# Kernel optimization log

Measured on AMD Instinct MI355X. Metric: run time of the kernel, lower is better.

Reference implementation:

```python
import jax, jax.numpy as jnp
import numpy as np

COMMITMENT_COST = 0.25


def setup_inputs() -> dict:
    key = jax.random.key(0)
    k1, k2 = jax.random.split(key)
    B, H, W, D, K = 64, 32, 32, 64, 1024
    x = jax.random.normal(k1, (B, H, W, D), dtype=jnp.float32)
    # variance_scaling(fan_in=D, uniform) ~ U(-sqrt(3/D), sqrt(3/D)); plain normal*scale is fine for a reference
    embeddings = jax.random.uniform(k2, (D, K), dtype=jnp.float32,
                                    minval=-np.sqrt(3.0 / D), maxval=np.sqrt(3.0 / D))
    return {"x": x, "embeddings": embeddings}


def reference(x, embeddings):
    D = embeddings.shape[0]
    K = embeddings.shape[1]
    flat = x.reshape(-1, D)                                   # [N, D]
    # squared euclidean distance: ||f||^2 - 2 f.E + ||e||^2 -> [N, K]
    distance = (jnp.sum(flat ** 2, axis=1, keepdims=True)
                - 2.0 * jnp.matmul(flat, embeddings)
                + jnp.sum(embeddings ** 2, axis=0, keepdims=True))
    encoding_indices_flat = jnp.argmax(-distance, axis=1)     # [N]
    encodings = jax.nn.one_hot(encoding_indices_flat, K, dtype=distance.dtype)  # [N, K]
    encoding_indices = encoding_indices_flat.reshape(x.shape[:-1])
    # quantize: gather rows of E^T -> same shape as x
    quantized = jnp.take(embeddings.T, encoding_indices, axis=0)
    e_latent_loss = jnp.mean((jax.lax.stop_gradient(quantized) - x) ** 2)
    q_latent_loss = jnp.mean((quantized - jax.lax.stop_gradient(x)) ** 2)
    loss = q_latent_loss + COMMITMENT_COST * e_latent_loss
    quantized_st = x + jax.lax.stop_gradient(quantized - x)   # straight-through
    avg_probs = jnp.mean(encodings, axis=0)                   # [K]
    perplexity = jnp.exp(-jnp.sum(avg_probs * jnp.log(avg_probs + 1e-10)))
    return quantized_st, loss, perplexity, encoding_indices
```

## Files before the change

### kernel.cpp

```cpp
#include <hip/hip_runtime.h>
#include <math.h>


typedef __attribute__((ext_vector_type(8))) short short8v;
typedef __attribute__((ext_vector_type(4))) float float4v;
typedef unsigned short u16;
typedef unsigned int u32;

constexpr int D = 64;
constexpr int K = 1024;
constexpr int NPTS = 65536;
constexpr long QOFF = (long)NPTS * D;
constexpr float BIAS = 24.0f;
constexpr float GATE = 5e-3f;

constexpr size_t OFF_LOSS = 0;
constexpr size_t OFF_CNT  = 256;
constexpr size_t OFF_EC   = OFF_CNT + 4096;
constexpr size_t OFF_ECB  = OFF_EC + 4096;
constexpr size_t OFF_ET   = OFF_ECB + 4096;
constexpr size_t OFF_H2   = OFF_ET + (size_t)K * D * 4;
constexpr size_t OFF_L2   = OFF_H2 + (size_t)K * D * 2;
constexpr size_t WS_ZERO  = OFF_CNT + 4096;

__device__ __forceinline__ float med3(float a, float b, float c) {
  return __builtin_amdgcn_fmed3f(a, b, c);
}
__device__ __forceinline__ u16 bf16rtn(float x) {
  u32 u = __float_as_uint(x);
  return (u16)((u + 0x7fffu + ((u >> 16) & 1u)) >> 16);
}
__device__ __forceinline__ float bf2f(u16 h) {
  return __uint_as_float(((u32)h) << 16);
}

__global__ __launch_bounds__(256) void prep_norm(const float* __restrict__ E,
                                                 float* __restrict__ eC,
                                                 float* __restrict__ eCb) {
  int k = blockIdx.x * 256 + threadIdx.x;
  float c = __fmul_rn(E[k], E[k]);
#pragma unroll
  for (int d = 1; d < D; ++d) {
    float v = E[d * K + k];
    c = __fadd_rn(c, __fmul_rn(v, v));
  }
  eC[k] = c;
  eCb[k] = c + BIAS;
}

__global__ __launch_bounds__(256) void prep_conv(const float* __restrict__ E,
                                                 float* __restrict__ Et,
                                                 u16* __restrict__ h2,
                                                 u16* __restrict__ l2) {
  int gid = blockIdx.x * 256 + threadIdx.x;
  int k = gid & 1023;
  int dg = gid >> 10;
#pragma unroll
  for (int i = 0; i < 4; ++i) {
    int d = dg * 4 + i;
    float v = E[d * K + k];
    Et[(size_t)k * 64 + d] = v;
    float m2 = -2.0f * v;
    u16 h = bf16rtn(m2);
    u16 l = bf16rtn(m2 - bf2f(h));
    h2[(size_t)k * 64 + d] = h;
    l2[(size_t)k * 64 + d] = l;
  }
}

__global__ __launch_bounds__(256) void vq_main(const float* __restrict__ x,
                                               const float* __restrict__ E,
                                               const u16* __restrict__ h2g,
                                               const u16* __restrict__ l2g,
                                               const float* __restrict__ eC,
                                               const float* __restrict__ eCb,
                                               const float* __restrict__ Etg,
                                               float* __restrict__ out,
                                               double* __restrict__ lossSum,
                                               int* __restrict__ counts) {
  __shared__ __align__(16) u16 hA[128 * 72];
  __shared__ __align__(16) u16 lA[128 * 72];
  __shared__ __align__(16) float ecb[128];
  __shared__ __align__(16) float topbuf[256 * 4];
  __shared__ int bkbuf[128];

  const int tid = threadIdx.x;
  const int w = tid >> 6;
  const int lane = tid & 63;
  const int col = lane & 15;
  const int quad = lane >> 4;
  const int blockBase = blockIdx.x * 128;
  const float INF = __builtin_inff();

  short8v Bh[2][2], Bl[2][2];
#pragma unroll
  for (int pt = 0; pt < 2; ++pt) {
    const float* xp = x + (size_t)(blockBase + w * 32 + pt * 16 + col) * 64;
#pragma unroll
    for (int s = 0; s < 2; ++s) {
      const float4* src = (const float4*)(xp + s * 32 + quad * 8);
      float4 a = src[0], b = src[1];
      float xs[8] = {a.x, a.y, a.z, a.w, b.x, b.y, b.z, b.w};
      short8v hf, lf;
#pragma unroll
      for (int j = 0; j < 8; ++j) {
        u16 h = bf16rtn(xs[j]);
        hf[j] = (short)h;
        lf[j] = (short)bf16rtn(xs[j] - bf2f(h));
      }
      Bh[pt][s] = hf;
      Bl[pt][s] = lf;
    }
  }

  float b1[2] = {INF, INF}, b2[2] = {INF, INF};

  for (int ch = 0; ch < 8; ++ch) {
    const int kbase = ch * 128;
    __syncthreads();
#pragma unroll
    for (int i = 0; i < 4; ++i) {
      int idx = tid + i * 256;
      int k = idx >> 3, dg = idx & 7;
      *(float4*)&hA[k * 72 + dg * 8] =
          *(const float4*)&h2g[(size_t)(kbase + k) * 64 + dg * 8];
      *(float4*)&lA[k * 72 + dg * 8] =
          *(const float4*)&l2g[(size_t)(kbase + k) * 64 + dg * 8];
    }
    if (tid < 32) *(float4*)&ecb[tid * 4] = *(const float4*)&eCb[kbase + tid * 4];
    __syncthreads();

#pragma unroll
    for (int ct = 0; ct < 8; ++ct) {
      const int rowbase = (ct * 16 + col) * 72;
      short8v Ah0 = *(const short8v*)&hA[rowbase + quad * 8];
      short8v Ah1 = *(const short8v*)&hA[rowbase + 32 + quad * 8];
      short8v Al0 = *(const short8v*)&lA[rowbase + quad * 8];
      short8v Al1 = *(const short8v*)&lA[rowbase + 32 + quad * 8];
      float4v Ci = *(const float4v*)&ecb[ct * 16 + quad * 4];
#pragma unroll
      for (int pt = 0; pt < 2; ++pt) {
        float4v C = Ci;
        C = __builtin_amdgcn_mfma_f32_16x16x32_bf16(Ah0, Bh[pt][0], C, 0, 0, 0);
        C = __builtin_amdgcn_mfma_f32_16x16x32_bf16(Ah1, Bh[pt][1], C, 0, 0, 0);
        C = __builtin_amdgcn_mfma_f32_16x16x32_bf16(Al0, Bh[pt][0], C, 0, 0, 0);
        C = __builtin_amdgcn_mfma_f32_16x16x32_bf16(Al1, Bh[pt][1], C, 0, 0, 0);
        C = __builtin_amdgcn_mfma_f32_16x16x32_bf16(Ah0, Bl[pt][0], C, 0, 0, 0);
        C = __builtin_amdgcn_mfma_f32_16x16x32_bf16(Ah1, Bl[pt][1], C, 0, 0, 0);
#pragma unroll
        for (int r = 0; r < 4; ++r) {
          u32 u = (__float_as_uint(C[r]) & 0xffffff00u) |
                  (u32)(ch * 32 + ct * 4 + r);
          float v = __uint_as_float(u);
          float pb = b1[pt];
          b1[pt] = fminf(pb, v);
          b2[pt] = med3(pb, b2[pt], v);
        }
      }
    }
  }

  topbuf[tid * 4 + 0] = b1[0];
  topbuf[tid * 4 + 1] = b2[0];
  topbuf[tid * 4 + 2] = b1[1];
  topbuf[tid * 4 + 3] = b2[1];
  __syncthreads();

  if (tid < 128) {
    const int mw = tid >> 5, mpt = (tid >> 4) & 1, mcol = tid & 15;
    float cv[8];
    int cq[8];
    float mv0 = INF, mv1 = INF;
    int q0 = 0;
#pragma unroll
    for (int q = 0; q < 4; ++q) {
      int lbase = (mw * 64 + q * 16 + mcol) * 4 + mpt * 2;
#pragma unroll
      for (int j = 0; j < 2; ++j) {
        float v = topbuf[lbase + j];
        cv[q * 2 + j] = v;
        cq[q * 2 + j] = q;
        if (v < mv0) { mv1 = mv0; mv0 = v; q0 = q; }
        else if (v < mv1) { mv1 = v; }
      }
    }
    u32 lb = __float_as_uint(mv0) & 255u;
    int bestk = (int)((lb >> 5) * 128 + ((lb >> 2) & 7) * 16 + q0 * 4 + (lb & 3));

    if (mv1 - mv0 < GATE) {
      const float* f = x + (size_t)(blockBase + tid) * 64;
      float r8[8];
#pragma unroll
      for (int j = 0; j < 8; ++j) { float fv = f[j]; r8[j] = __fmul_rn(fv, fv); }
#pragma unroll
      for (int i = 8; i < D; i += 8)
#pragma unroll
        for (int j = 0; j < 8; ++j) {
          float fv = f[i + j];
          r8[j] = __fadd_rn(r8[j], __fmul_rn(fv, fv));
        }
      float A = __fadd_rn(__fadd_rn(__fadd_rn(r8[0], r8[1]), __fadd_rn(r8[2], r8[3])),
                          __fadd_rn(__fadd_rn(r8[4], r8[5]), __fadd_rn(r8[6], r8[7])));
      float bd = INF;
      int bkk = K;
#pragma unroll
      for (int c = 0; c < 8; ++c) {
        u32 cb = __float_as_uint(cv[c]) & 255u;
        int k = (int)((cb >> 5) * 128 + ((cb >> 2) & 7) * 16 + cq[c] * 4 + (cb & 3));
        float m = 0.f;
#pragma unroll
        for (int d = 0; d < D; ++d) m = __fmaf_rn(f[d], E[d * K + k], m);
        float dist = __fadd_rn(__fsub_rn(A, __fmul_rn(2.f, m)), eC[k]);
        bool better = (dist < bd) || (dist == bd && k < bkk);
        bd = better ? dist : bd;
        bkk = better ? k : bkk;
      }
      bestk = bkk;
    }

    bkbuf[tid] = bestk;
    out[QOFF + 2 + blockBase + tid] = (float)bestk;
    atomicAdd(&counts[bestk], 1);
  }
  __syncthreads();

  const int pp = tid >> 1, half = tid & 1;
  const int bk = bkbuf[pp];
  const float4* et = (const float4*)(Etg + (size_t)bk * 64 + half * 32);
  const float4* xr = (const float4*)(x + (size_t)(blockBase + pp) * 64 + half * 32);
  float4* ov = (float4*)(out + (size_t)(blockBase + pp) * 64 + half * 32);
  float errs = 0.f;
#pragma unroll
  for (int i = 0; i < 8; ++i) {
    float4 qv = et[i];
    float4 xv = xr[i];
    float dx;
    dx = qv.x - xv.x; errs = fmaf(dx, dx, errs);
    dx = qv.y - xv.y; errs = fmaf(dx, dx, errs);
    dx = qv.z - xv.z; errs = fmaf(dx, dx, errs);
    dx = qv.w - xv.w; errs = fmaf(dx, dx, errs);
    ov[i] = qv;
  }
  double de = (double)errs;
#pragma unroll
  for (int off = 32; off > 0; off >>= 1) de += __shfl_down(de, off, 64);
  if (lane == 0) atomicAdd(lossSum, de);
}

__global__ __launch_bounds__(256) void vq_finalize(const double* __restrict__ lossSum,
                                                   const int* __restrict__ counts,
                                                   float* __restrict__ out) {
  __shared__ double sh[256];
  double ent = 0.0;
  for (int k = threadIdx.x; k < K; k += 256) {
    double pp = (double)counts[k] / (double)NPTS;
    ent += pp * log(pp + 1e-10);
  }
  sh[threadIdx.x] = ent;
  __syncthreads();
  for (int s = 128; s > 0; s >>= 1) {
    if (threadIdx.x < s) sh[threadIdx.x] += sh[threadIdx.x + s];
    __syncthreads();
  }
  if (threadIdx.x == 0) {
    out[QOFF + 0] = (float)(1.25 * (*lossSum) / (double)((long)NPTS * D));
    out[QOFF + 1] = (float)exp(-sh[0]);
  }
}

extern "C" void kernel_launch(void* const* d_in, const int* in_sizes, int n_in,
                              void* d_out, int out_size, void* d_ws, size_t ws_size,
                              hipStream_t stream) {
  const float* x = (const float*)d_in[0];
  const float* E = (const float*)d_in[1];
  float* out = (float*)d_out;

  char* ws = (char*)d_ws;
  double* lossSum = (double*)(ws + OFF_LOSS);
  int* counts = (int*)(ws + OFF_CNT);
  float* eC = (float*)(ws + OFF_EC);
  float* eCb = (float*)(ws + OFF_ECB);
  float* Etg = (float*)(ws + OFF_ET);
  u16* h2g = (u16*)(ws + OFF_H2);
  u16* l2g = (u16*)(ws + OFF_L2);

  hipMemsetAsync(d_ws, 0, WS_ZERO, stream);

  prep_norm<<<K / 256, 256, 0, stream>>>(E, eC, eCb);
  prep_conv<<<(K * 16) / 256, 256, 0, stream>>>(E, Etg, h2g, l2g);
  vq_main<<<NPTS / 128, 256, 0, stream>>>(x, E, h2g, l2g, eC, eCb, Etg, out,
                                          lossSum, counts);
  vq_finalize<<<1, 256, 0, stream>>>(lossSum, counts, out);
}
```

Baseline: 134.7 us.

## Use single fp16 MFMA pass with wider rescoring gate, drop LDS staging

Replaces the split bf16 hi/lo three-term product (6 MFMAs per tile) with a single fp16 product (2 MFMAs). The top-2 rescoring gate is widened to absorb the larger rounding error. Codebook tiles are now read straight from global/L2 instead of being staged through LDS with barriers, and the two prep kernels are merged into one. This cuts matrix-core work, LDS traffic and a kernel launch. The risk is more exact-rescore fallbacks and less coalesced per-lane global loads.

```diff
diff --git a/kernel.cpp b/kernel.cpp
--- a/kernel.cpp
+++ b/kernel.cpp
@@ -2,7 +2,7 @@
 #include <math.h>
 
 
-typedef __attribute__((ext_vector_type(8))) short short8v;
+typedef __attribute__((ext_vector_type(8))) _Float16 half8v;
 typedef __attribute__((ext_vector_type(4))) float float4v;
 typedef unsigned short u16;
 typedef unsigned int u32;
@@ -12,75 +12,58 @@
 constexpr int NPTS = 65536;
 constexpr long QOFF = (long)NPTS * D;
 constexpr float BIAS = 24.0f;
-constexpr float GATE = 5e-3f;
+constexpr float GATE = 2e-2f;
 
 constexpr size_t OFF_LOSS = 0;
 constexpr size_t OFF_CNT  = 256;
-constexpr size_t OFF_EC   = OFF_CNT + 4096;
-constexpr size_t OFF_ECB  = OFF_EC + 4096;
-constexpr size_t OFF_ET   = OFF_ECB + 4096;
-constexpr size_t OFF_H2   = OFF_ET + (size_t)K * D * 4;
-constexpr size_t OFF_L2   = OFF_H2 + (size_t)K * D * 2;
-constexpr size_t WS_ZERO  = OFF_CNT + 4096;
+constexpr size_t OFF_EC   = 4352;
+constexpr size_t OFF_ECB  = 8448;
+constexpr size_t OFF_ET   = 12544;
+constexpr size_t OFF_H16  = OFF_ET + (size_t)K * D * 4;
+constexpr size_t WS_ZERO  = 4352;
 
 __device__ __forceinline__ float med3(float a, float b, float c) {
   return __builtin_amdgcn_fmed3f(a, b, c);
 }
-__device__ __forceinline__ u16 bf16rtn(float x) {
-  u32 u = __float_as_uint(x);
-  return (u16)((u + 0x7fffu + ((u >> 16) & 1u)) >> 16);
-}
-__device__ __forceinline__ float bf2f(u16 h) {
-  return __uint_as_float(((u32)h) << 16);
-}
-
-__global__ __launch_bounds__(256) void prep_norm(const float* __restrict__ E,
-                                                 float* __restrict__ eC,
-                                                 float* __restrict__ eCb) {
-  int k = blockIdx.x * 256 + threadIdx.x;
-  float c = __fmul_rn(E[k], E[k]);
-#pragma unroll
-  for (int d = 1; d < D; ++d) {
-    float v = E[d * K + k];
-    c = __fadd_rn(c, __fmul_rn(v, v));
-  }
-  eC[k] = c;
-  eCb[k] = c + BIAS;
-}
-
-__global__ __launch_bounds__(256) void prep_conv(const float* __restrict__ E,
-                                                 float* __restrict__ Et,
-                                                 u16* __restrict__ h2,
-                                                 u16* __restrict__ l2) {
-  int gid = blockIdx.x * 256 + threadIdx.x;
-  int k = gid & 1023;
-  int dg = gid >> 10;
-#pragma unroll
-  for (int i = 0; i < 4; ++i) {
-    int d = dg * 4 + i;
-    float v = E[d * K + k];
-    Et[(size_t)k * 64 + d] = v;
-    float m2 = -2.0f * v;
-    u16 h = bf16rtn(m2);
-    u16 l = bf16rtn(m2 - bf2f(h));
-    h2[(size_t)k * 64 + d] = h;
-    l2[(size_t)k * 64 + d] = l;
+
+__global__ __launch_bounds__(256) void prep(const float* __restrict__ E,
+                                            float* __restrict__ eC,
+                                            float* __restrict__ eCb,
+                                            float* __restrict__ Et,
+                                            _Float16* __restrict__ h16) {
+  const int gid = blockIdx.x * 256 + threadIdx.x;
+  const int d = gid >> 8;
+  const int k0 = (gid & 255) * 4;
+  float4 v = *(const float4*)&E[d * K + k0];
+  Et[(size_t)(k0 + 0) * 64 + d] = v.x;
+  Et[(size_t)(k0 + 1) * 64 + d] = v.y;
+  Et[(size_t)(k0 + 2) * 64 + d] = v.z;
+  Et[(size_t)(k0 + 3) * 64 + d] = v.w;
+  h16[(size_t)(k0 + 0) * 64 + d] = (_Float16)(-2.0f * v.x);
+  h16[(size_t)(k0 + 1) * 64 + d] = (_Float16)(-2.0f * v.y);
+  h16[(size_t)(k0 + 2) * 64 + d] = (_Float16)(-2.0f * v.z);
+  h16[(size_t)(k0 + 3) * 64 + d] = (_Float16)(-2.0f * v.w);
+  if (gid < K) {
+    float c = __fmul_rn(E[gid], E[gid]);
+#pragma unroll
+    for (int dd = 1; dd < D; ++dd) {
+      float e = E[dd * K + gid];
+      c = __fadd_rn(c, __fmul_rn(e, e));
+    }
+    eC[gid] = c;
+    eCb[gid] = c + BIAS;
   }
 }
 
 __global__ __launch_bounds__(256) void vq_main(const float* __restrict__ x,
                                                const float* __restrict__ E,
-                                               const u16* __restrict__ h2g,
-                                               const u16* __restrict__ l2g,
+                                               const _Float16* __restrict__ h16,
                                                const float* __restrict__ eC,
                                                const float* __restrict__ eCb,
                                                const float* __restrict__ Etg,
                                                float* __restrict__ out,
                                                double* __restrict__ lossSum,
                                                int* __restrict__ counts) {
-  __shared__ __align__(16) u16 hA[128 * 72];
-  __shared__ __align__(16) u16 lA[128 * 72];
-  __shared__ __align__(16) float ecb[128];
   __shared__ __align__(16) float topbuf[256 * 4];
   __shared__ int bkbuf[128];
 
@@ -92,7 +75,7 @@
   const int blockBase = blockIdx.x * 128;
   const float INF = __builtin_inff();
 
-  short8v Bh[2][2], Bl[2][2];
+  half8v Bf[2][2];
 #pragma unroll
   for (int pt = 0; pt < 2; ++pt) {
     const float* xp = x + (size_t)(blockBase + w * 32 + pt * 16 + col) * 64;
@@ -100,53 +83,31 @@
     for (int s = 0; s < 2; ++s) {
       const float4* src = (const float4*)(xp + s * 32 + quad * 8);
       float4 a = src[0], b = src[1];
-      float xs[8] = {a.x, a.y, a.z, a.w, b.x, b.y, b.z, b.w};
-      short8v hf, lf;
-#pragma unroll
-      for (int j = 0; j < 8; ++j) {
-        u16 h = bf16rtn(xs[j]);
-        hf[j] = (short)h;
-        lf[j] = (short)bf16rtn(xs[j] - bf2f(h));
-      }
-      Bh[pt][s] = hf;
-      Bl[pt][s] = lf;
+      half8v hf;
+      hf[0] = (_Float16)a.x; hf[1] = (_Float16)a.y;
+      hf[2] = (_Float16)a.z; hf[3] = (_Float16)a.w;
+      hf[4] = (_Float16)b.x; hf[5] = (_Float16)b.y;
+      hf[6] = (_Float16)b.z; hf[7] = (_Float16)b.w;
+      Bf[pt][s] = hf;
     }
   }
 
   float b1[2] = {INF, INF}, b2[2] = {INF, INF};
 
+#pragma unroll 2
   for (int ch = 0; ch < 8; ++ch) {
-    const int kbase = ch * 128;
-    __syncthreads();
-#pragma unroll
-    for (int i = 0; i < 4; ++i) {
-      int idx = tid + i * 256;
-      int k = idx >> 3, dg = idx & 7;
-      *(float4*)&hA[k * 72 + dg * 8] =
-          *(const float4*)&h2g[(size_t)(kbase + k) * 64 + dg * 8];
-      *(float4*)&lA[k * 72 + dg * 8] =
-          *(const float4*)&l2g[(size_t)(kbase + k) * 64 + dg * 8];
-    }
-    if (tid < 32) *(float4*)&ecb[tid * 4] = *(const float4*)&eCb[kbase + tid * 4];
-    __syncthreads();
-
 #pragma unroll
     for (int ct = 0; ct < 8; ++ct) {
-      const int rowbase = (ct * 16 + col) * 72;
-      short8v Ah0 = *(const short8v*)&hA[rowbase + quad * 8];
-      short8v Ah1 = *(const short8v*)&hA[rowbase + 32 + quad * 8];
-      short8v Al0 = *(const short8v*)&lA[rowbase + quad * 8];
-      short8v Al1 = *(const short8v*)&lA[rowbase + 32 + quad * 8];
-      float4v Ci = *(const float4v*)&ecb[ct * 16 + quad * 4];
+      const int krow = ch * 128 + ct * 16;
+      const _Float16* arow = h16 + (size_t)(krow + col) * 64 + quad * 8;
+      half8v A0 = *(const half8v*)arow;
+      half8v A1 = *(const half8v*)(arow + 32);
+      float4v Ci = *(const float4v*)&eCb[krow + quad * 4];
 #pragma unroll
       for (int pt = 0; pt < 2; ++pt) {
         float4v C = Ci;
-        C = __builtin_amdgcn_mfma_f32_16x16x32_bf16(Ah0, Bh[pt][0], C, 0, 0, 0);
-        C = __builtin_amdgcn_mfma_f32_16x16x32_bf16(Ah1, Bh[pt][1], C, 0, 0, 0);
-        C = __builtin_amdgcn_mfma_f32_16x16x32_bf16(Al0, Bh[pt][0], C, 0, 0, 0);
-        C = __builtin_amdgcn_mfma_f32_16x16x32_bf16(Al1, Bh[pt][1], C, 0, 0, 0);
-        C = __builtin_amdgcn_mfma_f32_16x16x32_bf16(Ah0, Bl[pt][0], C, 0, 0, 0);
-        C = __builtin_amdgcn_mfma_f32_16x16x32_bf16(Ah1, Bl[pt][1], C, 0, 0, 0);
+        C = __builtin_amdgcn_mfma_f32_16x16x32_f16(A0, Bf[pt][0], C, 0, 0, 0);
+        C = __builtin_amdgcn_mfma_f32_16x16x32_f16(A1, Bf[pt][1], C, 0, 0, 0);
 #pragma unroll
         for (int r = 0; r < 4; ++r) {
           u32 u = (__float_as_uint(C[r]) & 0xffffff00u) |
@@ -281,14 +242,12 @@
   float* eC = (float*)(ws + OFF_EC);
   float* eCb = (float*)(ws + OFF_ECB);
   float* Etg = (float*)(ws + OFF_ET);
-  u16* h2g = (u16*)(ws + OFF_H2);
-  u16* l2g = (u16*)(ws + OFF_L2);
+  _Float16* h16 = (_Float16*)(ws + OFF_H16);
 
   hipMemsetAsync(d_ws, 0, WS_ZERO, stream);
 
-  prep_norm<<<K / 256, 256, 0, stream>>>(E, eC, eCb);
-  prep_conv<<<(K * 16) / 256, 256, 0, stream>>>(E, Etg, h2g, l2g);
-  vq_main<<<NPTS / 128, 256, 0, stream>>>(x, E, h2g, l2g, eC, eCb, Etg, out,
+  prep<<<64, 256, 0, stream>>>(E, eC, eCb, Etg, h16);
+  vq_main<<<NPTS / 128, 256, 0, stream>>>(x, E, h16, eC, eCb, Etg, out,
                                           lossSum, counts);
   vq_finalize<<<1, 256, 0, stream>>>(lossSum, counts, out);
 }
```

Measured after the change: 171.4 us. 27.3% more time.

## Merge prep kernels and fold finalize into main via last-block atomic

Applied to the files above, without the earlier changes.

Combines the two codebook preparation kernels into one that reads E with float4 loads. It removes the separate finalize launch: each block bumps a done counter, and the last block computes the entropy/perplexity and the loss output. The exact-rescoring fallback now loads the point into registers once and reads codebook rows from the transposed Et copy instead of strided E columns. The aim is fewer kernel launches and cheaper tie-break rescoring, at the cost of a grid-completion atomic and a serial tail in the last block.

```diff
diff --git a/kernel.cpp b/kernel.cpp
--- a/kernel.cpp
+++ b/kernel.cpp
@@ -13,15 +13,17 @@
 constexpr long QOFF = (long)NPTS * D;
 constexpr float BIAS = 24.0f;
 constexpr float GATE = 5e-3f;
+constexpr int GRID = 512;
 
 constexpr size_t OFF_LOSS = 0;
-constexpr size_t OFF_CNT  = 256;
-constexpr size_t OFF_EC   = OFF_CNT + 4096;
-constexpr size_t OFF_ECB  = OFF_EC + 4096;
-constexpr size_t OFF_ET   = OFF_ECB + 4096;
+constexpr size_t OFF_DONE = 8;
+constexpr size_t OFF_CNT  = 16;
+constexpr size_t WS_ZERO  = 4112;
+constexpr size_t OFF_EC   = 4352;
+constexpr size_t OFF_ECB  = 8448;
+constexpr size_t OFF_ET   = 12544;
 constexpr size_t OFF_H2   = OFF_ET + (size_t)K * D * 4;
 constexpr size_t OFF_L2   = OFF_H2 + (size_t)K * D * 2;
-constexpr size_t WS_ZERO  = OFF_CNT + 4096;
 
 __device__ __forceinline__ float med3(float a, float b, float c) {
   return __builtin_amdgcn_fmed3f(a, b, c);
@@ -34,55 +36,55 @@
   return __uint_as_float(((u32)h) << 16);
 }
 
-__global__ __launch_bounds__(256) void prep_norm(const float* __restrict__ E,
-                                                 float* __restrict__ eC,
-                                                 float* __restrict__ eCb) {
-  int k = blockIdx.x * 256 + threadIdx.x;
-  float c = __fmul_rn(E[k], E[k]);
-#pragma unroll
-  for (int d = 1; d < D; ++d) {
-    float v = E[d * K + k];
-    c = __fadd_rn(c, __fmul_rn(v, v));
-  }
-  eC[k] = c;
-  eCb[k] = c + BIAS;
-}
-
-__global__ __launch_bounds__(256) void prep_conv(const float* __restrict__ E,
-                                                 float* __restrict__ Et,
-                                                 u16* __restrict__ h2,
-                                                 u16* __restrict__ l2) {
-  int gid = blockIdx.x * 256 + threadIdx.x;
-  int k = gid & 1023;
-  int dg = gid >> 10;
+__global__ __launch_bounds__(256) void prep(const float* __restrict__ E,
+                                            float* __restrict__ eC,
+                                            float* __restrict__ eCb,
+                                            float* __restrict__ Et,
+                                            u16* __restrict__ h2,
+                                            u16* __restrict__ l2) {
+  const int gid = blockIdx.x * 256 + threadIdx.x;
+  const int d = gid >> 8;
+  const int k0 = (gid & 255) * 4;
+  float4 v = *(const float4*)&E[d * K + k0];
 #pragma unroll
   for (int i = 0; i < 4; ++i) {
-    int d = dg * 4 + i;
-    float v = E[d * K + k];
-    Et[(size_t)k * 64 + d] = v;
-    float m2 = -2.0f * v;
+    int k = k0 + i;
+    float e = (i == 0) ? v.x : (i == 1) ? v.y : (i == 2) ? v.z : v.w;
+    Et[(size_t)k * 64 + d] = e;
+    float m2 = -2.0f * e;
     u16 h = bf16rtn(m2);
-    u16 l = bf16rtn(m2 - bf2f(h));
     h2[(size_t)k * 64 + d] = h;
-    l2[(size_t)k * 64 + d] = l;
+    l2[(size_t)k * 64 + d] = bf16rtn(m2 - bf2f(h));
+  }
+  if (gid < K) {
+    float c = __fmul_rn(E[gid], E[gid]);
+#pragma unroll
+    for (int dd = 1; dd < D; ++dd) {
+      float e = E[dd * K + gid];
+      c = __fadd_rn(c, __fmul_rn(e, e));
+    }
+    eC[gid] = c;
+    eCb[gid] = c + BIAS;
   }
 }
 
 __global__ __launch_bounds__(256) void vq_main(const float* __restrict__ x,
-                                               const float* __restrict__ E,
                                                const u16* __restrict__ h2g,
                                                const u16* __restrict__ l2g,
                                                const float* __restrict__ eC,
-                                               const float* __restrict__ eCb,
+                                               const float* __restrict__ eCbG,
                                                const float* __restrict__ Etg,
                                                float* __restrict__ out,
                                                double* __restrict__ lossSum,
-                                               int* __restrict__ counts) {
+                                               int* __restrict__ counts,
+                                               int* __restrict__ done) {
   __shared__ __align__(16) u16 hA[128 * 72];
   __shared__ __align__(16) u16 lA[128 * 72];
   __shared__ __align__(16) float ecb[128];
   __shared__ __align__(16) float topbuf[256 * 4];
   __shared__ int bkbuf[128];
+  __shared__ double shred[256];
+  __shared__ int lastFlag;
 
   const int tid = threadIdx.x;
   const int w = tid >> 6;
@@ -127,7 +129,7 @@
       *(float4*)&lA[k * 72 + dg * 8] =
           *(const float4*)&l2g[(size_t)(kbase + k) * 64 + dg * 8];
     }
-    if (tid < 32) *(float4*)&ecb[tid * 4] = *(const float4*)&eCb[kbase + tid * 4];
+    if (tid < 32) *(float4*)&ecb[tid * 4] = *(const float4*)&eCbG[kbase + tid * 4];
     __syncthreads();
 
 #pragma unroll
@@ -188,28 +190,41 @@
     int bestk = (int)((lb >> 5) * 128 + ((lb >> 2) & 7) * 16 + q0 * 4 + (lb & 3));
 
     if (mv1 - mv0 < GATE) {
-      const float* f = x + (size_t)(blockBase + tid) * 64;
+      const float4* fx = (const float4*)(x + (size_t)(blockBase + tid) * 64);
+      float fr[64];
+#pragma unroll
+      for (int i = 0; i < 16; ++i) {
+        float4 v = fx[i];
+        fr[4 * i + 0] = v.x; fr[4 * i + 1] = v.y;
+        fr[4 * i + 2] = v.z; fr[4 * i + 3] = v.w;
+      }
       float r8[8];
 #pragma unroll
-      for (int j = 0; j < 8; ++j) { float fv = f[j]; r8[j] = __fmul_rn(fv, fv); }
+      for (int j = 0; j < 8; ++j) r8[j] = __fmul_rn(fr[j], fr[j]);
 #pragma unroll
       for (int i = 8; i < D; i += 8)
 #pragma unroll
-        for (int j = 0; j < 8; ++j) {
-          float fv = f[i + j];
-          r8[j] = __fadd_rn(r8[j], __fmul_rn(fv, fv));
-        }
+        for (int j = 0; j < 8; ++j)
+          r8[j] = __fadd_rn(r8[j], __fmul_rn(fr[i + j], fr[i + j]));
       float A = __fadd_rn(__fadd_rn(__fadd_rn(r8[0], r8[1]), __fadd_rn(r8[2], r8[3])),
                           __fadd_rn(__fadd_rn(r8[4], r8[5]), __fadd_rn(r8[6], r8[7])));
+
       float bd = INF;
       int bkk = K;
 #pragma unroll
       for (int c = 0; c < 8; ++c) {
         u32 cb = __float_as_uint(cv[c]) & 255u;
         int k = (int)((cb >> 5) * 128 + ((cb >> 2) & 7) * 16 + cq[c] * 4 + (cb & 3));
+        const float4* er = (const float4*)(Etg + (size_t)k * 64);
         float m = 0.f;
 #pragma unroll
-        for (int d = 0; d < D; ++d) m = __fmaf_rn(f[d], E[d * K + k], m);
+        for (int i = 0; i < 16; ++i) {
+          float4 e = er[i];
+          m = __fmaf_rn(fr[4 * i + 0], e.x, m);
+          m = __fmaf_rn(fr[4 * i + 1], e.y, m);
+          m = __fmaf_rn(fr[4 * i + 2], e.z, m);
+          m = __fmaf_rn(fr[4 * i + 3], e.w, m);
+        }
         float dist = __fadd_rn(__fsub_rn(A, __fmul_rn(2.f, m)), eC[k]);
         bool better = (dist < bd) || (dist == bd && k < bkk);
         bd = better ? dist : bd;
@@ -245,26 +260,34 @@
 #pragma unroll
   for (int off = 32; off > 0; off >>= 1) de += __shfl_down(de, off, 64);
   if (lane == 0) atomicAdd(lossSum, de);
-}
-
-__global__ __launch_bounds__(256) void vq_finalize(const double* __restrict__ lossSum,
-                                                   const int* __restrict__ counts,
-                                                   float* __restrict__ out) {
-  __shared__ double sh[256];
-  double ent = 0.0;
-  for (int k = threadIdx.x; k < K; k += 256) {
-    double pp = (double)counts[k] / (double)NPTS;
-    ent += pp * log(pp + 1e-10);
-  }
-  sh[threadIdx.x] = ent;
+
   __syncthreads();
-  for (int s = 128; s > 0; s >>= 1) {
-    if (threadIdx.x < s) sh[threadIdx.x] += sh[threadIdx.x + s];
+  if (tid == 0) {
+    int old = __hip_atomic_fetch_add(done, 1, __ATOMIC_ACQ_REL,
+                                     __HIP_MEMORY_SCOPE_AGENT);
+    lastFlag = (old == GRID - 1);
+  }
+  __syncthreads();
+  if (lastFlag) {
+    double ent = 0.0;
+    for (int k = tid; k < K; k += 256) {
+      int c = __hip_atomic_load(&counts[k], __ATOMIC_RELAXED,
+                                __HIP_MEMORY_SCOPE_AGENT);
+      double pp2 = (double)c / (double)NPTS;
+      ent += pp2 * log(pp2 + 1e-10);
+    }
+    shred[tid] = ent;
     __syncthreads();
-  }
-  if (threadIdx.x == 0) {
-    out[QOFF + 0] = (float)(1.25 * (*lossSum) / (double)((long)NPTS * D));
-    out[QOFF + 1] = (float)exp(-sh[0]);
+    for (int s = 128; s > 0; s >>= 1) {
+      if (tid < s) shred[tid] += shred[tid + s];
+      __syncthreads();
+    }
+    if (tid == 0) {
+      double ls = __hip_atomic_load(lossSum, __ATOMIC_RELAXED,
+                                    __HIP_MEMORY_SCOPE_AGENT);
+      out[QOFF + 0] = (float)(1.25 * ls / (double)((long)NPTS * D));
+      out[QOFF + 1] = (float)exp(-shred[0]);
+    }
   }
 }
 
@@ -277,6 +300,7 @@
 
   char* ws = (char*)d_ws;
   double* lossSum = (double*)(ws + OFF_LOSS);
+  int* done = (int*)(ws + OFF_DONE);
   int* counts = (int*)(ws + OFF_CNT);
   float* eC = (float*)(ws + OFF_EC);
   float* eCb = (float*)(ws + OFF_ECB);
@@ -286,9 +310,7 @@
 
   hipMemsetAsync(d_ws, 0, WS_ZERO, stream);
 
-  prep_norm<<<K / 256, 256, 0, stream>>>(E, eC, eCb);
-  prep_conv<<<(K * 16) / 256, 256, 0, stream>>>(E, Etg, h2g, l2g);
-  vq_main<<<NPTS / 128, 256, 0, stream>>>(x, E, h2g, l2g, eC, eCb, Etg, out,
-                                          lossSum, counts);
-  vq_finalize<<<1, 256, 0, stream>>>(lossSum, counts, out);
-}
+  prep<<<64, 256, 0, stream>>>(E, eC, eCb, Etg, h2g, l2g);
+  vq_main<<<GRID, 256, 0, stream>>>(x, h2g, l2g, eC, eCb, Etg, out, lossSum,
+                                    counts, done);
+}
```

New measurement: 142.6 us. +5.9%, slower.
